# Optimization experiments

Measured on AMD Instinct MI355X. Metric: run time of the kernel, lower is better.

## Reference

```python
import jax, jax.numpy as jnp
import numpy as np

N = 50000   # num_nodes
E = 400000  # random edges (avg degree 8)


def setup_inputs() -> dict:
    key = jax.random.key(0)
    ks = jax.random.split(key, 12)

    def w(k, shape):
        # xavier-ish scaling
        return (jax.random.normal(k, shape, jnp.float32)
                / jnp.sqrt(jnp.float32(shape[0])))

    return {
        "node_emb": jax.random.normal(ks[0], (N, 128), jnp.float32) * 0.05,
        "edge_index": jax.random.randint(ks[1], (2, E), 0, N, dtype=jnp.int32),
        "W1": w(ks[2], (128, 512)), "b1": jnp.zeros((512,), jnp.float32),
        "W2": w(ks[3], (512, 128)), "b2": jnp.zeros((128,), jnp.float32),
        "Wres": w(ks[4], (512, 128)), "bres": jnp.zeros((128,), jnp.float32),
        "Wfc1": w(ks[5], (128, 256)), "bfc1": jnp.zeros((256,), jnp.float32),
        "Wfc2": w(ks[6], (256, 1)), "bfc2": jnp.zeros((1,), jnp.float32),
    }


def reference(node_emb, edge_index, W1, b1, W2, b2, Wres, bres,
              Wfc1, bfc1, Wfc2, bfc2):
    n = node_emb.shape[0]
    loops = jnp.arange(n, dtype=edge_index.dtype)
    # explicit add_self_loops in forward + GCNConv's internal gcn_norm self
    # loops => each node gets TWO self loops (faithful to the torch code).
    src = jnp.concatenate([edge_index[0], loops, loops])
    dst = jnp.concatenate([edge_index[1], loops, loops])

    deg = jax.ops.segment_sum(jnp.ones(src.shape, node_emb.dtype), dst,
                              num_segments=n)
    dinv = jnp.where(deg > 0, jax.lax.rsqrt(deg), 0.0)
    norm = dinv[src] * dinv[dst]  # [Etot]

    def gcn(x, W, b):
        h = x @ W                                    # [N, out]
        msg = h[src] * norm[:, None]                 # gather + scale
        agg = jax.ops.segment_sum(msg, dst, num_segments=n)  # scatter-add
        return agg + b

    x1 = jax.nn.relu(gcn(node_emb, W1, b1))   # [N, 512] (dropout = eval/id)
    x2 = jax.nn.relu(gcn(x1, W2, b2))          # [N, 128]
    x = x2 + x1 @ Wres + bres                  # residual projection
    A = jax.nn.relu(x @ Wfc1 + bfc1) @ Wfc2 + bfc2  # [N, 1]
    return (x, A)
```

## Files before the change

### kernel.cpp

```cpp
#include <hip/hip_runtime.h>


typedef unsigned short u16;
typedef short bf16x8 __attribute__((ext_vector_type(8)));
typedef unsigned short us8 __attribute__((ext_vector_type(8)));
typedef float f32x4 __attribute__((ext_vector_type(4)));

static inline int cdiv_ll(long long a, long long b) { return (int)((a + b - 1) / b); }

__device__ inline float bf2f(u16 u) {
    union { unsigned int i; float f; } v; v.i = ((unsigned int)u) << 16; return v.f;
}
__device__ inline u16 f2bf(float x) {
    union { float f; unsigned int i; } v; v.f = x;
    unsigned int r = v.i + 0x7fffu + ((v.i >> 16) & 1u);
    return (u16)(r >> 16);
}


__global__ __launch_bounds__(256) void setup_kernel(const float* __restrict__ emb,
                                                    const float* __restrict__ W1,
                                                    const float* __restrict__ W2,
                                                    const float* __restrict__ Wres,
                                                    const float* __restrict__ Wfc1,
                                                    const float* __restrict__ bfc2,
                                                    u16* __restrict__ embb,
                                                    u16* __restrict__ W1t,
                                                    u16* __restrict__ Wct,
                                                    u16* __restrict__ Wfc1t,
                                                    int* __restrict__ cnt,
                                                    float* __restrict__ Aout,
                                                    int N) {
    long long r = (long long)blockIdx.x * 256 + threadIdx.x;
    const long long nf2b = (long long)N * 32;
    if (r < nf2b) {
        float4 v = ((const float4*)emb)[r];
        uint2 o;
        o.x = (unsigned)f2bf(v.x) | ((unsigned)f2bf(v.y) << 16);
        o.y = (unsigned)f2bf(v.z) | ((unsigned)f2bf(v.w) << 16);
        ((uint2*)embb)[r] = o;
        return;
    }
    r -= nf2b;
    if (r < 512 * 128) {
        int n = (int)(r / 128), k = (int)(r % 128);
        W1t[r] = f2bf(W1[(size_t)k * 512 + n]);
        return;
    }
    r -= 512 * 128;
    if (r < 256 * 512) {
        int n = (int)(r / 512), k = (int)(r % 512);
        float v = (n < 128) ? W2[(size_t)k * 128 + n] : Wres[(size_t)k * 128 + (n - 128)];
        Wct[r] = f2bf(v);
        return;
    }
    r -= 256 * 512;
    if (r < 256 * 128) {
        int n = (int)(r / 128), k = (int)(r % 128);
        Wfc1t[r] = f2bf(Wfc1[(size_t)k * 256 + n]);
        return;
    }
    r -= 256 * 128;
    if (r < N) { cnt[(int)r] = 0; return; }
    r -= N;
    if (r < N) Aout[(int)r] = bfc2[0];
}


__global__ __launch_bounds__(256) void hist_kernel(const int* __restrict__ dst,
                                                   int* __restrict__ cnt, int E) {
    int e = blockIdx.x * 256 + threadIdx.x;
    if (e < E) atomicAdd(&cnt[dst[e]], 1);
}

__global__ __launch_bounds__(256) void scanA_kernel(const int* __restrict__ cnt,
                                                    int* __restrict__ excl,
                                                    int* __restrict__ bsum, int N) {
    __shared__ int tmp[256];
    int i = blockIdx.x * 256 + threadIdx.x;
    int v = (i < N) ? cnt[i] : 0;
    tmp[threadIdx.x] = v;
    __syncthreads();
    for (int o = 1; o < 256; o <<= 1) {
        int t = (threadIdx.x >= (unsigned)o) ? tmp[threadIdx.x - o] : 0;
        __syncthreads();
        tmp[threadIdx.x] += t;
        __syncthreads();
    }
    if (i < N) excl[i] = tmp[threadIdx.x] - v;
    if (threadIdx.x == 255) bsum[blockIdx.x] = tmp[255];
}

__global__ __launch_bounds__(256) void scanB_kernel(int* __restrict__ bsum, int nb) {
    __shared__ int tmp[256];
    int v = (threadIdx.x < (unsigned)nb) ? bsum[threadIdx.x] : 0;
    tmp[threadIdx.x] = v;
    __syncthreads();
    for (int o = 1; o < 256; o <<= 1) {
        int t = (threadIdx.x >= (unsigned)o) ? tmp[threadIdx.x - o] : 0;
        __syncthreads();
        tmp[threadIdx.x] += t;
        __syncthreads();
    }
    if (threadIdx.x < (unsigned)nb) bsum[threadIdx.x] = tmp[threadIdx.x] - v;
}

__global__ __launch_bounds__(256) void scanC_kernel(const int* __restrict__ excl,
                                                    const int* __restrict__ bsum,
                                                    const int* __restrict__ cnt,
                                                    int* __restrict__ rowptr,
                                                    int* __restrict__ cursor,
                                                    float* __restrict__ dinv,
                                                    int N, int E) {
    int i = blockIdx.x * 256 + threadIdx.x;
    if (i < N) {
        int r = excl[i] + bsum[blockIdx.x];
        rowptr[i] = r;
        cursor[i] = r;
        dinv[i] = rsqrtf((float)cnt[i] + 2.0f);
    }
    if (i == 0) rowptr[N] = E;
}

__global__ __launch_bounds__(256) void fill_kernel(const int* __restrict__ src,
                                                   const int* __restrict__ dst,
                                                   const float* __restrict__ dinv,
                                                   int* __restrict__ cursor,
                                                   int* __restrict__ csr_src,
                                                   float* __restrict__ csr_w, int E) {
    int e = blockIdx.x * 256 + threadIdx.x;
    if (e >= E) return;
    int s = src[e], d = dst[e];
    int idx = atomicAdd(&cursor[d], 1);
    csr_src[idx] = s;
    csr_w[idx] = dinv[s] * dinv[d];
}


#define AGG_EDGE(SR, WR)                                                       \
    {                                                                          \
        unsigned int vv = hp[(size_t)(SR) * 64 + lane];                        \
        ax = fmaf(bf2f((u16)vv), (WR), ax);                                    \
        ay = fmaf(bf2f((u16)(vv >> 16)), (WR), ay);                            \
    }

__device__ inline void agg_row(const unsigned int* __restrict__ hp,
                               const int* __restrict__ rowptr,
                               const int* __restrict__ csr_src,
                               const float* __restrict__ csr_w,
                               const float* __restrict__ dinv,
                               int wid, int lane, float& ax, float& ay) {
    float dv = dinv[wid];
    unsigned int hv = hp[(size_t)wid * 64 + lane];
    float c0 = 2.0f * dv * dv;
    ax = bf2f((u16)hv) * c0;
    ay = bf2f((u16)(hv >> 16)) * c0;
    int e = rowptr[wid], e1 = rowptr[wid + 1];
    for (; e + 7 < e1; e += 8) {
        int s0 = csr_src[e + 0], s1 = csr_src[e + 1], s2 = csr_src[e + 2], s3 = csr_src[e + 3];
        int s4 = csr_src[e + 4], s5 = csr_src[e + 5], s6 = csr_src[e + 6], s7 = csr_src[e + 7];
        float w0 = csr_w[e + 0], w1 = csr_w[e + 1], w2 = csr_w[e + 2], w3 = csr_w[e + 3];
        float w4 = csr_w[e + 4], w5 = csr_w[e + 5], w6 = csr_w[e + 6], w7 = csr_w[e + 7];
        AGG_EDGE(s0, w0); AGG_EDGE(s1, w1); AGG_EDGE(s2, w2); AGG_EDGE(s3, w3);
        AGG_EDGE(s4, w4); AGG_EDGE(s5, w5); AGG_EDGE(s6, w6); AGG_EDGE(s7, w7);
    }
    if (e + 3 < e1) {
        int s0 = csr_src[e + 0], s1 = csr_src[e + 1], s2 = csr_src[e + 2], s3 = csr_src[e + 3];
        float w0 = csr_w[e + 0], w1 = csr_w[e + 1], w2 = csr_w[e + 2], w3 = csr_w[e + 3];
        AGG_EDGE(s0, w0); AGG_EDGE(s1, w1); AGG_EDGE(s2, w2); AGG_EDGE(s3, w3);
        e += 4;
    }
    for (; e < e1; ++e) {
        int s0 = csr_src[e]; float w0 = csr_w[e];
        AGG_EDGE(s0, w0);
    }
}

__global__ __launch_bounds__(256) void aggb_kernel(const u16* __restrict__ hb,
                                                   const int* __restrict__ rowptr,
                                                   const int* __restrict__ csr_src,
                                                   const float* __restrict__ csr_w,
                                                   const float* __restrict__ dinv,
                                                   u16* __restrict__ out, int N) {
    int wid  = (blockIdx.x * blockDim.x + threadIdx.x) >> 6;
    int lane = threadIdx.x & 63;
    if (wid >= N) return;
    float ax, ay;
    agg_row((const unsigned int*)hb, rowptr, csr_src, csr_w, dinv, wid, lane, ax, ay);
    ((unsigned int*)out)[(size_t)wid * 64 + lane] =
        (unsigned)f2bf(ax) | ((unsigned)f2bf(ay) << 16);
}

__global__ __launch_bounds__(256) void aggfin_kernel(const u16* __restrict__ hb,
                                                     const int* __restrict__ rowptr,
                                                     const int* __restrict__ csr_src,
                                                     const float* __restrict__ csr_w,
                                                     const float* __restrict__ dinv,
                                                     const float* __restrict__ b2,
                                                     const float* __restrict__ bres,
                                                     float* __restrict__ xout,
                                                     u16* __restrict__ xb, int N) {
    int wid  = (blockIdx.x * blockDim.x + threadIdx.x) >> 6;
    int lane = threadIdx.x & 63;
    if (wid >= N) return;
    float ax, ay;
    agg_row((const unsigned int*)hb, rowptr, csr_src, csr_w, dinv, wid, lane, ax, ay);
    float2 bb = ((const float2*)b2)[lane];
    float2 rr = ((const float2*)bres)[lane];
    float2 hres = ((float2*)xout)[(size_t)wid * 64 + lane];
    float ox = fmaxf(ax + bb.x, 0.f) + hres.x + rr.x;
    float oy = fmaxf(ay + bb.y, 0.f) + hres.y + rr.y;
    ((float2*)xout)[(size_t)wid * 64 + lane] = make_float2(ox, oy);
    ((unsigned int*)xb)[(size_t)wid * 64 + lane] =
        (unsigned)f2bf(ox) | ((unsigned)f2bf(oy) << 16);
}


template <int MODE, int PIPE>
__global__ __launch_bounds__(512) void mgemm(const u16* __restrict__ A,
                                             const u16* __restrict__ Bt,
                                             int M, int Nn, int K,
                                             const float* __restrict__ bias,
                                             u16* __restrict__ Cb,
                                             float* __restrict__ Cf,
                                             const float* __restrict__ w2) {
    __shared__ u16 As[128][72];
    __shared__ u16 Bs[256][72];
    const int t = threadIdx.x;
    const int bm = blockIdx.y * 128;
    const int bn = blockIdx.x * 256;
    const int w = t >> 6, lane = t & 63;
    const int wm = w >> 2, wn = w & 3;
    const int l15 = lane & 15, lg = lane >> 4;
    const int srow = t >> 3, scol = (t & 7) * 8;

    f32x4 acc[4][4];
#pragma unroll
    for (int i = 0; i < 4; ++i)
#pragma unroll
        for (int j = 0; j < 4; ++j) acc[i][j] = (f32x4)(0.0f);

    us8 ra[2], rb[4];
    if (PIPE) {
#pragma unroll
        for (int i = 0; i < 2; ++i) {
            int row = srow + 64 * i;
            us8 v = (us8)(u16)0;
            if (bm + row < M) v = *(const us8*)(A + (size_t)(bm + row) * K + scol);
            ra[i] = v;
        }
#pragma unroll
        for (int i = 0; i < 4; ++i)
            rb[i] = *(const us8*)(Bt + (size_t)(bn + srow + 64 * i) * K + scol);
    }

    for (int kk = 0; kk < K; kk += 64) {
        if (PIPE) {
#pragma unroll
            for (int i = 0; i < 2; ++i) *(us8*)&As[srow + 64 * i][scol] = ra[i];
#pragma unroll
            for (int i = 0; i < 4; ++i) *(us8*)&Bs[srow + 64 * i][scol] = rb[i];
        } else {
#pragma unroll
            for (int i = 0; i < 2; ++i) {
                int row = srow + 64 * i;
                us8 v = (us8)(u16)0;
                if (bm + row < M)
                    v = *(const us8*)(A + (size_t)(bm + row) * K + kk + scol);
                *(us8*)&As[row][scol] = v;
            }
#pragma unroll
            for (int i = 0; i < 4; ++i) {
                int row = srow + 64 * i;
                *(us8*)&Bs[row][scol] =
                    *(const us8*)(Bt + (size_t)(bn + row) * K + kk + scol);
            }
        }
        __syncthreads();

        if (PIPE && kk + 64 < K) {
#pragma unroll
            for (int i = 0; i < 2; ++i) {
                int row = srow + 64 * i;
                us8 v = (us8)(u16)0;
                if (bm + row < M)
                    v = *(const us8*)(A + (size_t)(bm + row) * K + kk + 64 + scol);
                ra[i] = v;
            }
#pragma unroll
            for (int i = 0; i < 4; ++i)
                rb[i] = *(const us8*)(Bt + (size_t)(bn + srow + 64 * i) * K + kk + 64 + scol);
        }

#pragma unroll
        for (int ks = 0; ks < 2; ++ks) {
            const int ko = 32 * ks + lg * 8;
            bf16x8 bfr[4], afr[4];
#pragma unroll
            for (int fn = 0; fn < 4; ++fn)
                bfr[fn] = *(const bf16x8*)&Bs[64 * wn + 16 * fn + l15][ko];
#pragma unroll
            for (int fm = 0; fm < 4; ++fm)
                afr[fm] = *(const bf16x8*)&As[64 * wm + 16 * fm + l15][ko];
#pragma unroll
            for (int fm = 0; fm < 4; ++fm)
#pragma unroll
                for (int fn = 0; fn < 4; ++fn)
                    acc[fm][fn] = __builtin_amdgcn_mfma_f32_16x16x32_bf16(
                        bfr[fn], afr[fm], acc[fm][fn], 0, 0, 0);
        }
        __syncthreads();
    }

    if (MODE == 3) {
        float4 bl4[4], wl4[4];
#pragma unroll
        for (int fn = 0; fn < 4; ++fn) {
            int c = bn + 64 * wn + 16 * fn + 4 * lg;
            bl4[fn] = *(const float4*)&bias[c];
            wl4[fn] = *(const float4*)&w2[c];
        }
#pragma unroll
        for (int fm = 0; fm < 4; ++fm) {
            float p = 0.f;
#pragma unroll
            for (int fn = 0; fn < 4; ++fn) {
                p += fmaxf(acc[fm][fn][0] + bl4[fn].x, 0.f) * wl4[fn].x;
                p += fmaxf(acc[fm][fn][1] + bl4[fn].y, 0.f) * wl4[fn].y;
                p += fmaxf(acc[fm][fn][2] + bl4[fn].z, 0.f) * wl4[fn].z;
                p += fmaxf(acc[fm][fn][3] + bl4[fn].w, 0.f) * wl4[fn].w;
            }
            p += __shfl_xor(p, 16);
            p += __shfl_xor(p, 32);
            int row = bm + 64 * wm + 16 * fm + l15;
            if (lane < 16 && row < M) atomicAdd(&Cf[row], p);
        }
        return;
    }

#pragma unroll
    for (int fm = 0; fm < 4; ++fm) {
        const int row = bm + 64 * wm + 16 * fm + l15;
        if (row >= M) continue;
#pragma unroll
        for (int fn = 0; fn < 4; ++fn) {
            const int col = bn + 64 * wn + 16 * fn + 4 * lg;
            f32x4 v = acc[fm][fn];
            if (MODE == 1) {
                float4 b4 = *(const float4*)&bias[col];
                float v0 = fmaxf(v[0] + b4.x, 0.f), v1 = fmaxf(v[1] + b4.y, 0.f);
                float v2 = fmaxf(v[2] + b4.z, 0.f), v3 = fmaxf(v[3] + b4.w, 0.f);
                uint2 o;
                o.x = (unsigned)f2bf(v0) | ((unsigned)f2bf(v1) << 16);
                o.y = (unsigned)f2bf(v2) | ((unsigned)f2bf(v3) << 16);
                *(uint2*)(Cb + (size_t)row * Nn + col) = o;
            } else {
                if (col < 128) {
                    uint2 o;
                    o.x = (unsigned)f2bf(v[0]) | ((unsigned)f2bf(v[1]) << 16);
                    o.y = (unsigned)f2bf(v[2]) | ((unsigned)f2bf(v[3]) << 16);
                    *(uint2*)(Cb + (size_t)row * 128 + col) = o;
                } else {
                    *(float4*)(Cf + (size_t)row * 128 + (col - 128)) =
                        make_float4(v[0], v[1], v[2], v[3]);
                }
            }
        }
    }
}


extern "C" void kernel_launch(void* const* d_in, const int* in_sizes, int n_in,
                              void* d_out, int out_size, void* d_ws, size_t ws_size,
                              hipStream_t stream) {
    const float* emb  = (const float*)d_in[0];
    const int*   eidx = (const int*)d_in[1];
    const float* W1   = (const float*)d_in[2];
    const float* b1   = (const float*)d_in[3];
    const float* W2   = (const float*)d_in[4];
    const float* b2   = (const float*)d_in[5];
    const float* Wres = (const float*)d_in[6];
    const float* bres = (const float*)d_in[7];
    const float* Wfc1 = (const float*)d_in[8];
    const float* bfc1 = (const float*)d_in[9];
    const float* Wfc2 = (const float*)d_in[10];
    const float* bfc2 = (const float*)d_in[11];

    const int N = in_sizes[0] / 128;
    const int E = in_sizes[1] / 2;
    const int* srcv = eidx;
    const int* dstv = eidx + E;

    float* out  = (float*)d_out;
    float* xout = out;
    float* Aout = out + (size_t)N * 128;

    char* p = (char*)d_ws;
    float* dinv  = (float*)p;            p += (size_t)N * 4;
    float* csr_w = (float*)p;            p += (size_t)E * 4;
    u16*  embb   = (u16*)p;              p += (size_t)N * 128 * 2;
    u16*  aggEb  = (u16*)p;              p += (size_t)N * 128 * 2;
    u16*  x1b    = (u16*)p;              p += (size_t)N * 512 * 2;
    u16*  h2b    = (u16*)p;              p += (size_t)N * 128 * 2;
    u16*  xb     = (u16*)p;              p += (size_t)N * 128 * 2;
    u16*  W1t    = (u16*)p;              p += (size_t)512 * 128 * 2;
    u16*  Wct    = (u16*)p;              p += (size_t)256 * 512 * 2;
    u16*  Wfc1t  = (u16*)p;              p += (size_t)256 * 128 * 2;
    int*  cnt     = (int*)p;             p += (size_t)N * 4;
    int*  excl    = (int*)p;             p += (size_t)N * 4;
    int*  rowptr  = (int*)p;             p += (size_t)(N + 1) * 4;
    int*  cursor  = (int*)p;             p += (size_t)N * 4;
    int*  bsum    = (int*)p;             p += 256 * 4;
    int*  csr_src = (int*)p;             p += (size_t)E * 4;

    const int T  = 256;
    const int nb = cdiv_ll(N, 256);

    const long long setup_work = (long long)N * 32 + 512 * 128 + 256 * 512
                               + 256 * 128 + (long long)N + (long long)N;
    setup_kernel<<<cdiv_ll(setup_work, T), T, 0, stream>>>(
        emb, W1, W2, Wres, Wfc1, bfc2, embb, W1t, Wct, Wfc1t, cnt, Aout, N);

    hist_kernel<<<cdiv_ll(E, T), T, 0, stream>>>(dstv, cnt, E);
    scanA_kernel<<<nb, T, 0, stream>>>(cnt, excl, bsum, N);
    scanB_kernel<<<1, T, 0, stream>>>(bsum, nb);
    scanC_kernel<<<nb, T, 0, stream>>>(excl, bsum, cnt, rowptr, cursor, dinv, N, E);
    fill_kernel<<<cdiv_ll(E, T), T, 0, stream>>>(srcv, dstv, dinv, cursor, csr_src, csr_w, E);

    aggb_kernel<<<cdiv_ll((long long)N * 64, T), T, 0, stream>>>(
        embb, rowptr, csr_src, csr_w, dinv, aggEb, N);

    mgemm<1, 0><<<dim3(512 / 256, cdiv_ll(N, 128)), 512, 0, stream>>>(
        aggEb, W1t, N, 512, 128, b1, x1b, nullptr, nullptr);

    mgemm<2, 1><<<dim3(1, cdiv_ll(N, 128)), 512, 0, stream>>>(
        x1b, Wct, N, 256, 512, nullptr, h2b, xout, nullptr);

    aggfin_kernel<<<cdiv_ll((long long)N * 64, T), T, 0, stream>>>(
        h2b, rowptr, csr_src, csr_w, dinv, b2, bres, xout, xb, N);

    mgemm<3, 0><<<dim3(1, cdiv_ll(N, 128)), 512, 0, stream>>>(
        xb, Wfc1t, N, 256, 128, bfc1, nullptr, Aout, Wfc2);
}
```

Measured before the change: 198.0 us.

## Chunk feature dimension into 32-column slabs for cache-friendly aggregation gathers

Stores the bf16 node features consumed by both aggregations in a chunked layout, [4][N][32], where each slab holds 32 features for every node. Each aggregation runs as 4 passes, one per slab, with 16 lanes per node. A slab is about 3.2 MB, so the random neighbour gathers in a pass stay within a smaller working set that fits in L2. Setup, the first GEMM's A-loader and the second GEMM's h2 epilogue are all changed to read or write the chunked layout. The cost is that every edge's index and weight is now read four times, and each gather is a shorter 64-byte segment.

```diff
diff --git a/kernel.cpp b/kernel.cpp
--- a/kernel.cpp
+++ b/kernel.cpp
@@ -34,11 +34,13 @@
     long long r = (long long)blockIdx.x * 256 + threadIdx.x;
     const long long nf2b = (long long)N * 32;
     if (r < nf2b) {
+        int node = (int)(r >> 5);
+        int f    = (int)(r & 31) * 4;
         float4 v = ((const float4*)emb)[r];
         uint2 o;
         o.x = (unsigned)f2bf(v.x) | ((unsigned)f2bf(v.y) << 16);
         o.y = (unsigned)f2bf(v.z) | ((unsigned)f2bf(v.w) << 16);
-        ((uint2*)embb)[r] = o;
+        *(uint2*)(embb + ((size_t)(f >> 5) * N + node) * 32 + (f & 31)) = o;
         return;
     }
     r -= nf2b;
@@ -137,86 +139,74 @@
 }
 
 
-#define AGG_EDGE(SR, WR)                                                       \
+#define AGGC_EDGE(SR, WR)                                                      \
     {                                                                          \
-        unsigned int vv = hp[(size_t)(SR) * 64 + lane];                        \
+        unsigned int vv = hp[(size_t)(SR) * 16 + l];                           \
         ax = fmaf(bf2f((u16)vv), (WR), ax);                                    \
         ay = fmaf(bf2f((u16)(vv >> 16)), (WR), ay);                            \
     }
 
-__device__ inline void agg_row(const unsigned int* __restrict__ hp,
-                               const int* __restrict__ rowptr,
-                               const int* __restrict__ csr_src,
-                               const float* __restrict__ csr_w,
-                               const float* __restrict__ dinv,
-                               int wid, int lane, float& ax, float& ay) {
-    float dv = dinv[wid];
-    unsigned int hv = hp[(size_t)wid * 64 + lane];
+template <int FINAL>
+__global__ __launch_bounds__(256) void aggc_kernel(const u16* __restrict__ hb,
+                                                   const int* __restrict__ rowptr,
+                                                   const int* __restrict__ csr_src,
+                                                   const float* __restrict__ csr_w,
+                                                   const float* __restrict__ dinv,
+                                                   const float* __restrict__ b2,
+                                                   const float* __restrict__ bres,
+                                                   float* __restrict__ xout,
+                                                   u16* __restrict__ outb,
+                                                   int N) {
+    const int l = threadIdx.x & 15;
+    const int node = blockIdx.x * 16 + (threadIdx.x >> 4);
+    const int chunk = blockIdx.y;
+    if (node >= N) return;
+    const unsigned int* hp = (const unsigned int*)hb + (size_t)chunk * N * 16;
+
+    float dv = dinv[node];
     float c0 = 2.0f * dv * dv;
-    ax = bf2f((u16)hv) * c0;
-    ay = bf2f((u16)(hv >> 16)) * c0;
-    int e = rowptr[wid], e1 = rowptr[wid + 1];
+    unsigned int hv = hp[(size_t)node * 16 + l];
+    float ax = bf2f((u16)hv) * c0;
+    float ay = bf2f((u16)(hv >> 16)) * c0;
+
+    int e = rowptr[node], e1 = rowptr[node + 1];
     for (; e + 7 < e1; e += 8) {
         int s0 = csr_src[e + 0], s1 = csr_src[e + 1], s2 = csr_src[e + 2], s3 = csr_src[e + 3];
         int s4 = csr_src[e + 4], s5 = csr_src[e + 5], s6 = csr_src[e + 6], s7 = csr_src[e + 7];
         float w0 = csr_w[e + 0], w1 = csr_w[e + 1], w2 = csr_w[e + 2], w3 = csr_w[e + 3];
         float w4 = csr_w[e + 4], w5 = csr_w[e + 5], w6 = csr_w[e + 6], w7 = csr_w[e + 7];
-        AGG_EDGE(s0, w0); AGG_EDGE(s1, w1); AGG_EDGE(s2, w2); AGG_EDGE(s3, w3);
-        AGG_EDGE(s4, w4); AGG_EDGE(s5, w5); AGG_EDGE(s6, w6); AGG_EDGE(s7, w7);
+        AGGC_EDGE(s0, w0); AGGC_EDGE(s1, w1); AGGC_EDGE(s2, w2); AGGC_EDGE(s3, w3);
+        AGGC_EDGE(s4, w4); AGGC_EDGE(s5, w5); AGGC_EDGE(s6, w6); AGGC_EDGE(s7, w7);
     }
     if (e + 3 < e1) {
         int s0 = csr_src[e + 0], s1 = csr_src[e + 1], s2 = csr_src[e + 2], s3 = csr_src[e + 3];
         float w0 = csr_w[e + 0], w1 = csr_w[e + 1], w2 = csr_w[e + 2], w3 = csr_w[e + 3];
-        AGG_EDGE(s0, w0); AGG_EDGE(s1, w1); AGG_EDGE(s2, w2); AGG_EDGE(s3, w3);
+        AGGC_EDGE(s0, w0); AGGC_EDGE(s1, w1); AGGC_EDGE(s2, w2); AGGC_EDGE(s3, w3);
         e += 4;
     }
     for (; e < e1; ++e) {
         int s0 = csr_src[e]; float w0 = csr_w[e];
-        AGG_EDGE(s0, w0);
-    }
-}
-
-__global__ __launch_bounds__(256) void aggb_kernel(const u16* __restrict__ hb,
-                                                   const int* __restrict__ rowptr,
-                                                   const int* __restrict__ csr_src,
-                                                   const float* __restrict__ csr_w,
-                                                   const float* __restrict__ dinv,
-                                                   u16* __restrict__ out, int N) {
-    int wid  = (blockIdx.x * blockDim.x + threadIdx.x) >> 6;
-    int lane = threadIdx.x & 63;
-    if (wid >= N) return;
-    float ax, ay;
-    agg_row((const unsigned int*)hb, rowptr, csr_src, csr_w, dinv, wid, lane, ax, ay);
-    ((unsigned int*)out)[(size_t)wid * 64 + lane] =
-        (unsigned)f2bf(ax) | ((unsigned)f2bf(ay) << 16);
-}
-
-__global__ __launch_bounds__(256) void aggfin_kernel(const u16* __restrict__ hb,
-                                                     const int* __restrict__ rowptr,
-                                                     const int* __restrict__ csr_src,
-                                                     const float* __restrict__ csr_w,
-                                                     const float* __restrict__ dinv,
-                                                     const float* __restrict__ b2,
-                                                     const float* __restrict__ bres,
-                                                     float* __restrict__ xout,
-                                                     u16* __restrict__ xb, int N) {
-    int wid  = (blockIdx.x * blockDim.x + threadIdx.x) >> 6;
-    int lane = threadIdx.x & 63;
-    if (wid >= N) return;
-    float ax, ay;
-    agg_row((const unsigned int*)hb, rowptr, csr_src, csr_w, dinv, wid, lane, ax, ay);
-    float2 bb = ((const float2*)b2)[lane];
-    float2 rr = ((const float2*)bres)[lane];
-    float2 hres = ((float2*)xout)[(size_t)wid * 64 + lane];
-    float ox = fmaxf(ax + bb.x, 0.f) + hres.x + rr.x;
-    float oy = fmaxf(ay + bb.y, 0.f) + hres.y + rr.y;
-    ((float2*)xout)[(size_t)wid * 64 + lane] = make_float2(ox, oy);
-    ((unsigned int*)xb)[(size_t)wid * 64 + lane] =
-        (unsigned)f2bf(ox) | ((unsigned)f2bf(oy) << 16);
-}
-
-
-template <int MODE, int PIPE>
+        AGGC_EDGE(s0, w0);
+    }
+
+    if (FINAL) {
+        int f2 = chunk * 16 + l;
+        float2 bb = ((const float2*)b2)[f2];
+        float2 rr = ((const float2*)bres)[f2];
+        float2 hres = ((float2*)xout)[(size_t)node * 64 + f2];
+        float ox = fmaxf(ax + bb.x, 0.f) + hres.x + rr.x;
+        float oy = fmaxf(ay + bb.y, 0.f) + hres.y + rr.y;
+        ((float2*)xout)[(size_t)node * 64 + f2] = make_float2(ox, oy);
+        ((unsigned int*)outb)[(size_t)node * 64 + f2] =
+            (unsigned)f2bf(ox) | ((unsigned)f2bf(oy) << 16);
+    } else {
+        ((unsigned int*)outb)[((size_t)chunk * N + node) * 16 + l] =
+            (unsigned)f2bf(ax) | ((unsigned)f2bf(ay) << 16);
+    }
+}
+
+
+template <int MODE, int PIPE, int ACHUNK>
 __global__ __launch_bounds__(512) void mgemm(const u16* __restrict__ A,
                                              const u16* __restrict__ Bt,
                                              int M, int Nn, int K,
@@ -234,6 +224,13 @@
     const int l15 = lane & 15, lg = lane >> 4;
     const int srow = t >> 3, scol = (t & 7) * 8;
 
+    auto ald = [&](int grow, int col) -> us8 {
+        if (grow >= M) return (us8)(u16)0;
+        if (ACHUNK)
+            return *(const us8*)(A + ((size_t)(col >> 5) * M + grow) * 32 + (col & 31));
+        return *(const us8*)(A + (size_t)grow * K + col);
+    };
+
     f32x4 acc[4][4];
 #pragma unroll
     for (int i = 0; i < 4; ++i)
@@ -243,12 +240,7 @@
     us8 ra[2], rb[4];
     if (PIPE) {
 #pragma unroll
-        for (int i = 0; i < 2; ++i) {
-            int row = srow + 64 * i;
-            us8 v = (us8)(u16)0;
-            if (bm + row < M) v = *(const us8*)(A + (size_t)(bm + row) * K + scol);
-            ra[i] = v;
-        }
+        for (int i = 0; i < 2; ++i) ra[i] = ald(bm + srow + 64 * i, scol);
 #pragma unroll
         for (int i = 0; i < 4; ++i)
             rb[i] = *(const us8*)(Bt + (size_t)(bn + srow + 64 * i) * K + scol);
@@ -262,13 +254,8 @@
             for (int i = 0; i < 4; ++i) *(us8*)&Bs[srow + 64 * i][scol] = rb[i];
         } else {
 #pragma unroll
-            for (int i = 0; i < 2; ++i) {
-                int row = srow + 64 * i;
-                us8 v = (us8)(u16)0;
-                if (bm + row < M)
-                    v = *(const us8*)(A + (size_t)(bm + row) * K + kk + scol);
-                *(us8*)&As[row][scol] = v;
-            }
+            for (int i = 0; i < 2; ++i)
+                *(us8*)&As[srow + 64 * i][scol] = ald(bm + srow + 64 * i, kk + scol);
 #pragma unroll
             for (int i = 0; i < 4; ++i) {
                 int row = srow + 64 * i;
@@ -280,13 +267,7 @@
 
         if (PIPE && kk + 64 < K) {
 #pragma unroll
-            for (int i = 0; i < 2; ++i) {
-                int row = srow + 64 * i;
-                us8 v = (us8)(u16)0;
-                if (bm + row < M)
-                    v = *(const us8*)(A + (size_t)(bm + row) * K + kk + 64 + scol);
-                ra[i] = v;
-            }
+            for (int i = 0; i < 2; ++i) ra[i] = ald(bm + srow + 64 * i, kk + 64 + scol);
 #pragma unroll
             for (int i = 0; i < 4; ++i)
                 rb[i] = *(const us8*)(Bt + (size_t)(bn + srow + 64 * i) * K + kk + 64 + scol);
@@ -359,7 +340,7 @@
                     uint2 o;
                     o.x = (unsigned)f2bf(v[0]) | ((unsigned)f2bf(v[1]) << 16);
                     o.y = (unsigned)f2bf(v[2]) | ((unsigned)f2bf(v[3]) << 16);
-                    *(uint2*)(Cb + (size_t)row * 128 + col) = o;
+                    *(uint2*)(Cb + ((size_t)(col >> 5) * M + row) * 32 + (col & 31)) = o;
                 } else {
                     *(float4*)(Cf + (size_t)row * 128 + (col - 128)) =
                         make_float4(v[0], v[1], v[2], v[3]);
@@ -427,18 +408,19 @@
     scanC_kernel<<<nb, T, 0, stream>>>(excl, bsum, cnt, rowptr, cursor, dinv, N, E);
     fill_kernel<<<cdiv_ll(E, T), T, 0, stream>>>(srcv, dstv, dinv, cursor, csr_src, csr_w, E);
 
-    aggb_kernel<<<cdiv_ll((long long)N * 64, T), T, 0, stream>>>(
-        embb, rowptr, csr_src, csr_w, dinv, aggEb, N);
-
-    mgemm<1, 0><<<dim3(512 / 256, cdiv_ll(N, 128)), 512, 0, stream>>>(
+    dim3 aggGrid(cdiv_ll(N, 16), 4);
+    aggc_kernel<0><<<aggGrid, T, 0, stream>>>(
+        embb, rowptr, csr_src, csr_w, dinv, nullptr, nullptr, nullptr, aggEb, N);
+
+    mgemm<1, 0, 1><<<dim3(512 / 256, cdiv_ll(N, 128)), 512, 0, stream>>>(
         aggEb, W1t, N, 512, 128, b1, x1b, nullptr, nullptr);
 
-    mgemm<2, 1><<<dim3(1, cdiv_ll(N, 128)), 512, 0, stream>>>(
+    mgemm<2, 1, 0><<<dim3(1, cdiv_ll(N, 128)), 512, 0, stream>>>(
         x1b, Wct, N, 256, 512, nullptr, h2b, xout, nullptr);
 
-    aggfin_kernel<<<cdiv_ll((long long)N * 64, T), T, 0, stream>>>(
+    aggc_kernel<1><<<aggGrid, T, 0, stream>>>(
         h2b, rowptr, csr_src, csr_w, dinv, b2, bres, xout, xb, N);
 
-    mgemm<3, 0><<<dim3(1, cdiv_ll(N, 128)), 512, 0, stream>>>(
+    mgemm<3, 0, 0><<<dim3(1, cdiv_ll(N, 128)), 512, 0, stream>>>(
         xb, Wfc1t, N, 256, 128, bfc1, nullptr, Aout, Wfc2);
 }
```

Result: slower. 212.7 us (+7.4%).

## Fuse layer-1 GEMM into combined W2/Wres GEMM keeping x1 in LDS

Applied to the files above, without the earlier changes.

The first-layer GEMM (aggE·W1 + bias, relu) and the second GEMM (x1·[W2|Wres]) are merged into one kernel. Each block computes a 128x128 chunk of x1 in shared memory and immediately consumes it, so the N×512 bf16 x1 intermediate is never written to or read back from global memory. The scan kernels are also merged: each block reduces the preceding block sums itself, which removes the single-block scanB launch. The cost is about 136KB of dynamic LDS per block, which lowers occupancy, and there is no global-load pipelining in the fused loop.

```diff
diff --git a/kernel.cpp b/kernel.cpp
--- a/kernel.cpp
+++ b/kernel.cpp
@@ -91,30 +91,25 @@
     if (threadIdx.x == 255) bsum[blockIdx.x] = tmp[255];
 }
 
-__global__ __launch_bounds__(256) void scanB_kernel(int* __restrict__ bsum, int nb) {
+__global__ __launch_bounds__(256) void scanC2_kernel(const int* __restrict__ excl,
+                                                     const int* __restrict__ bsum,
+                                                     const int* __restrict__ cnt,
+                                                     int* __restrict__ rowptr,
+                                                     int* __restrict__ cursor,
+                                                     float* __restrict__ dinv,
+                                                     int N, int E) {
     __shared__ int tmp[256];
-    int v = (threadIdx.x < (unsigned)nb) ? bsum[threadIdx.x] : 0;
-    tmp[threadIdx.x] = v;
+    int t = threadIdx.x;
+    tmp[t] = (t < (int)blockIdx.x) ? bsum[t] : 0;
     __syncthreads();
-    for (int o = 1; o < 256; o <<= 1) {
-        int t = (threadIdx.x >= (unsigned)o) ? tmp[threadIdx.x - o] : 0;
-        __syncthreads();
-        tmp[threadIdx.x] += t;
-        __syncthreads();
-    }
-    if (threadIdx.x < (unsigned)nb) bsum[threadIdx.x] = tmp[threadIdx.x] - v;
-}
-
-__global__ __launch_bounds__(256) void scanC_kernel(const int* __restrict__ excl,
-                                                    const int* __restrict__ bsum,
-                                                    const int* __restrict__ cnt,
-                                                    int* __restrict__ rowptr,
-                                                    int* __restrict__ cursor,
-                                                    float* __restrict__ dinv,
-                                                    int N, int E) {
-    int i = blockIdx.x * 256 + threadIdx.x;
+    for (int o = 128; o; o >>= 1) {
+        if (t < o) tmp[t] += tmp[t + o];
+        __syncthreads();
+    }
+    int pre = tmp[0];
+    int i = blockIdx.x * 256 + t;
     if (i < N) {
-        int r = excl[i] + bsum[blockIdx.x];
+        int r = excl[i] + pre;
         rowptr[i] = r;
         cursor[i] = r;
         dinv[i] = rsqrtf((float)cnt[i] + 2.0f);
@@ -216,156 +211,219 @@
 }
 
 
-template <int MODE, int PIPE>
-__global__ __launch_bounds__(512) void mgemm(const u16* __restrict__ A,
-                                             const u16* __restrict__ Bt,
-                                             int M, int Nn, int K,
-                                             const float* __restrict__ bias,
-                                             u16* __restrict__ Cb,
-                                             float* __restrict__ Cf,
-                                             const float* __restrict__ w2) {
-    __shared__ u16 As[128][72];
-    __shared__ u16 Bs[256][72];
+__global__ __launch_bounds__(512) void mgemm12(const u16* __restrict__ aggE,
+                                               const u16* __restrict__ W1t,
+                                               const u16* __restrict__ Wct,
+                                               const float* __restrict__ b1,
+                                               int M,
+                                               u16* __restrict__ h2b,
+                                               float* __restrict__ xout) {
+    extern __shared__ u16 smem[];
+    u16* Ag  = smem;
+    u16* Ws  = Ag + 128 * 136;
+    u16* X1s = Ws + 256 * 136;
+    const int LD = 136;
+
     const int t = threadIdx.x;
-    const int bm = blockIdx.y * 128;
-    const int bn = blockIdx.x * 256;
+    const int bm = blockIdx.x * 128;
     const int w = t >> 6, lane = t & 63;
     const int wm = w >> 2, wn = w & 3;
     const int l15 = lane & 15, lg = lane >> 4;
-    const int srow = t >> 3, scol = (t & 7) * 8;
-
-    f32x4 acc[4][4];
+
+#pragma unroll
+    for (int i = 0; i < 4; ++i) {
+        int c = t + 512 * i;
+        int row = c >> 4, cs = (c & 15) * 8;
+        us8 v = (us8)(u16)0;
+        if (bm + row < M) v = *(const us8*)(aggE + (size_t)(bm + row) * 128 + cs);
+        *(us8*)&Ag[row * LD + cs] = v;
+    }
+
+    f32x4 acc2[4][4];
 #pragma unroll
     for (int i = 0; i < 4; ++i)
 #pragma unroll
-        for (int j = 0; j < 4; ++j) acc[i][j] = (f32x4)(0.0f);
-
-    us8 ra[2], rb[4];
-    if (PIPE) {
-#pragma unroll
-        for (int i = 0; i < 2; ++i) {
-            int row = srow + 64 * i;
-            us8 v = (us8)(u16)0;
-            if (bm + row < M) v = *(const us8*)(A + (size_t)(bm + row) * K + scol);
-            ra[i] = v;
-        }
+        for (int j = 0; j < 4; ++j) acc2[i][j] = (f32x4)(0.0f);
+
+    for (int p = 0; p < 4; ++p) {
+        __syncthreads();
+#pragma unroll
+        for (int i = 0; i < 4; ++i) {
+            int c = t + 512 * i;
+            int row = c >> 4, cs = (c & 15) * 8;
+            *(us8*)&Ws[row * LD + cs] =
+                *(const us8*)(W1t + (size_t)(128 * p + row) * 128 + cs);
+        }
+        __syncthreads();
+
+        f32x4 acc1[4][2];
 #pragma unroll
         for (int i = 0; i < 4; ++i)
-            rb[i] = *(const us8*)(Bt + (size_t)(bn + srow + 64 * i) * K + scol);
-    }
-
-    for (int kk = 0; kk < K; kk += 64) {
-        if (PIPE) {
-#pragma unroll
-            for (int i = 0; i < 2; ++i) *(us8*)&As[srow + 64 * i][scol] = ra[i];
-#pragma unroll
-            for (int i = 0; i < 4; ++i) *(us8*)&Bs[srow + 64 * i][scol] = rb[i];
-        } else {
-#pragma unroll
-            for (int i = 0; i < 2; ++i) {
-                int row = srow + 64 * i;
-                us8 v = (us8)(u16)0;
-                if (bm + row < M)
-                    v = *(const us8*)(A + (size_t)(bm + row) * K + kk + scol);
-                *(us8*)&As[row][scol] = v;
-            }
-#pragma unroll
-            for (int i = 0; i < 4; ++i) {
-                int row = srow + 64 * i;
-                *(us8*)&Bs[row][scol] =
-                    *(const us8*)(Bt + (size_t)(bn + row) * K + kk + scol);
-            }
-        }
-        __syncthreads();
-
-        if (PIPE && kk + 64 < K) {
-#pragma unroll
-            for (int i = 0; i < 2; ++i) {
-                int row = srow + 64 * i;
-                us8 v = (us8)(u16)0;
-                if (bm + row < M)
-                    v = *(const us8*)(A + (size_t)(bm + row) * K + kk + 64 + scol);
-                ra[i] = v;
-            }
-#pragma unroll
-            for (int i = 0; i < 4; ++i)
-                rb[i] = *(const us8*)(Bt + (size_t)(bn + srow + 64 * i) * K + kk + 64 + scol);
-        }
-
-#pragma unroll
-        for (int ks = 0; ks < 2; ++ks) {
+#pragma unroll
+            for (int j = 0; j < 2; ++j) acc1[i][j] = (f32x4)(0.0f);
+#pragma unroll
+        for (int ks = 0; ks < 4; ++ks) {
             const int ko = 32 * ks + lg * 8;
-            bf16x8 bfr[4], afr[4];
-#pragma unroll
-            for (int fn = 0; fn < 4; ++fn)
-                bfr[fn] = *(const bf16x8*)&Bs[64 * wn + 16 * fn + l15][ko];
-#pragma unroll
-            for (int fm = 0; fm < 4; ++fm)
-                afr[fm] = *(const bf16x8*)&As[64 * wm + 16 * fm + l15][ko];
-#pragma unroll
-            for (int fm = 0; fm < 4; ++fm)
-#pragma unroll
-                for (int fn = 0; fn < 4; ++fn)
-                    acc[fm][fn] = __builtin_amdgcn_mfma_f32_16x16x32_bf16(
-                        bfr[fn], afr[fm], acc[fm][fn], 0, 0, 0);
-        }
-        __syncthreads();
-    }
-
-    if (MODE == 3) {
-        float4 bl4[4], wl4[4];
-#pragma unroll
-        for (int fn = 0; fn < 4; ++fn) {
-            int c = bn + 64 * wn + 16 * fn + 4 * lg;
-            bl4[fn] = *(const float4*)&bias[c];
-            wl4[fn] = *(const float4*)&w2[c];
-        }
+            bf16x8 wfr[2], afr[4];
+#pragma unroll
+            for (int fn = 0; fn < 2; ++fn)
+                wfr[fn] = *(const bf16x8*)&Ws[(32 * wn + 16 * fn + l15) * LD + ko];
+#pragma unroll
+            for (int fm = 0; fm < 4; ++fm)
+                afr[fm] = *(const bf16x8*)&Ag[(64 * wm + 16 * fm + l15) * LD + ko];
+#pragma unroll
+            for (int fm = 0; fm < 4; ++fm)
+#pragma unroll
+                for (int fn = 0; fn < 2; ++fn)
+                    acc1[fm][fn] = __builtin_amdgcn_mfma_f32_16x16x32_bf16(
+                        wfr[fn], afr[fm], acc1[fm][fn], 0, 0, 0);
+        }
+        __syncthreads();
+
 #pragma unroll
         for (int fm = 0; fm < 4; ++fm) {
-            float p = 0.f;
-#pragma unroll
-            for (int fn = 0; fn < 4; ++fn) {
-                p += fmaxf(acc[fm][fn][0] + bl4[fn].x, 0.f) * wl4[fn].x;
-                p += fmaxf(acc[fm][fn][1] + bl4[fn].y, 0.f) * wl4[fn].y;
-                p += fmaxf(acc[fm][fn][2] + bl4[fn].z, 0.f) * wl4[fn].z;
-                p += fmaxf(acc[fm][fn][3] + bl4[fn].w, 0.f) * wl4[fn].w;
-            }
-            p += __shfl_xor(p, 16);
-            p += __shfl_xor(p, 32);
-            int row = bm + 64 * wm + 16 * fm + l15;
-            if (lane < 16 && row < M) atomicAdd(&Cf[row], p);
-        }
-        return;
-    }
-
-#pragma unroll
-    for (int fm = 0; fm < 4; ++fm) {
-        const int row = bm + 64 * wm + 16 * fm + l15;
-        if (row >= M) continue;
-#pragma unroll
-        for (int fn = 0; fn < 4; ++fn) {
-            const int col = bn + 64 * wn + 16 * fn + 4 * lg;
-            f32x4 v = acc[fm][fn];
-            if (MODE == 1) {
-                float4 b4 = *(const float4*)&bias[col];
+#pragma unroll
+            for (int fn = 0; fn < 2; ++fn) {
+                int col1 = 32 * wn + 16 * fn + 4 * lg;
+                float4 b4 = *(const float4*)&b1[128 * p + col1];
+                f32x4 v = acc1[fm][fn];
                 float v0 = fmaxf(v[0] + b4.x, 0.f), v1 = fmaxf(v[1] + b4.y, 0.f);
                 float v2 = fmaxf(v[2] + b4.z, 0.f), v3 = fmaxf(v[3] + b4.w, 0.f);
                 uint2 o;
                 o.x = (unsigned)f2bf(v0) | ((unsigned)f2bf(v1) << 16);
                 o.y = (unsigned)f2bf(v2) | ((unsigned)f2bf(v3) << 16);
-                *(uint2*)(Cb + (size_t)row * Nn + col) = o;
+                *(uint2*)&X1s[(64 * wm + 16 * fm + l15) * LD + col1] = o;
+            }
+        }
+#pragma unroll
+        for (int i = 0; i < 8; ++i) {
+            int c = t + 512 * i;
+            int row = c >> 4, cs = (c & 15) * 8;
+            *(us8*)&Ws[row * LD + cs] =
+                *(const us8*)(Wct + (size_t)row * 512 + 128 * p + cs);
+        }
+        __syncthreads();
+
+#pragma unroll
+        for (int ks = 0; ks < 4; ++ks) {
+            const int ko = 32 * ks + lg * 8;
+            bf16x8 wfr[4], xfr[4];
+#pragma unroll
+            for (int fn = 0; fn < 4; ++fn)
+                wfr[fn] = *(const bf16x8*)&Ws[(64 * wn + 16 * fn + l15) * LD + ko];
+#pragma unroll
+            for (int fm = 0; fm < 4; ++fm)
+                xfr[fm] = *(const bf16x8*)&X1s[(64 * wm + 16 * fm + l15) * LD + ko];
+#pragma unroll
+            for (int fm = 0; fm < 4; ++fm)
+#pragma unroll
+                for (int fn = 0; fn < 4; ++fn)
+                    acc2[fm][fn] = __builtin_amdgcn_mfma_f32_16x16x32_bf16(
+                        wfr[fn], xfr[fm], acc2[fm][fn], 0, 0, 0);
+        }
+    }
+
+#pragma unroll
+    for (int fm = 0; fm < 4; ++fm) {
+        const int row = bm + 64 * wm + 16 * fm + l15;
+        if (row >= M) continue;
+#pragma unroll
+        for (int fn = 0; fn < 4; ++fn) {
+            const int col = 64 * wn + 16 * fn + 4 * lg;
+            f32x4 v = acc2[fm][fn];
+            if (col < 128) {
+                uint2 o;
+                o.x = (unsigned)f2bf(v[0]) | ((unsigned)f2bf(v[1]) << 16);
+                o.y = (unsigned)f2bf(v[2]) | ((unsigned)f2bf(v[3]) << 16);
+                *(uint2*)(h2b + (size_t)row * 128 + col) = o;
             } else {
-                if (col < 128) {
-                    uint2 o;
-                    o.x = (unsigned)f2bf(v[0]) | ((unsigned)f2bf(v[1]) << 16);
-                    o.y = (unsigned)f2bf(v[2]) | ((unsigned)f2bf(v[3]) << 16);
-                    *(uint2*)(Cb + (size_t)row * 128 + col) = o;
-                } else {
-                    *(float4*)(Cf + (size_t)row * 128 + (col - 128)) =
-                        make_float4(v[0], v[1], v[2], v[3]);
-                }
+                *(float4*)(xout + (size_t)row * 128 + (col - 128)) =
+                    make_float4(v[0], v[1], v[2], v[3]);
             }
         }
+    }
+}
+
+
+__global__ __launch_bounds__(512) void head_gemm(const u16* __restrict__ A,
+                                                 const u16* __restrict__ Bt,
+                                                 int M,
+                                                 const float* __restrict__ bias,
+                                                 const float* __restrict__ w2,
+                                                 float* __restrict__ Cf) {
+    __shared__ u16 As[128][72];
+    __shared__ u16 Bs[256][72];
+    const int t = threadIdx.x;
+    const int bm = blockIdx.x * 128;
+    const int w = t >> 6, lane = t & 63;
+    const int wm = w >> 2, wn = w & 3;
+    const int l15 = lane & 15, lg = lane >> 4;
+    const int srow = t >> 3, scol = (t & 7) * 8;
+    const int K = 128;
+
+    f32x4 acc[4][4];
+#pragma unroll
+    for (int i = 0; i < 4; ++i)
+#pragma unroll
+        for (int j = 0; j < 4; ++j) acc[i][j] = (f32x4)(0.0f);
+
+    for (int kk = 0; kk < K; kk += 64) {
+#pragma unroll
+        for (int i = 0; i < 2; ++i) {
+            int row = srow + 64 * i;
+            us8 v = (us8)(u16)0;
+            if (bm + row < M)
+                v = *(const us8*)(A + (size_t)(bm + row) * K + kk + scol);
+            *(us8*)&As[row][scol] = v;
+        }
+#pragma unroll
+        for (int i = 0; i < 4; ++i) {
+            int row = srow + 64 * i;
+            *(us8*)&Bs[row][scol] =
+                *(const us8*)(Bt + (size_t)row * K + kk + scol);
+        }
+        __syncthreads();
+#pragma unroll
+        for (int ks = 0; ks < 2; ++ks) {
+            const int ko = 32 * ks + lg * 8;
+            bf16x8 bfr[4], afr[4];
+#pragma unroll
+            for (int fn = 0; fn < 4; ++fn)
+                bfr[fn] = *(const bf16x8*)&Bs[64 * wn + 16 * fn + l15][ko];
+#pragma unroll
+            for (int fm = 0; fm < 4; ++fm)
+                afr[fm] = *(const bf16x8*)&As[64 * wm + 16 * fm + l15][ko];
+#pragma unroll
+            for (int fm = 0; fm < 4; ++fm)
+#pragma unroll
+                for (int fn = 0; fn < 4; ++fn)
+                    acc[fm][fn] = __builtin_amdgcn_mfma_f32_16x16x32_bf16(
+                        bfr[fn], afr[fm], acc[fm][fn], 0, 0, 0);
+        }
+        __syncthreads();
+    }
+
+    float4 bl4[4], wl4[4];
+#pragma unroll
+    for (int fn = 0; fn < 4; ++fn) {
+        int c = 64 * wn + 16 * fn + 4 * lg;
+        bl4[fn] = *(const float4*)&bias[c];
+        wl4[fn] = *(const float4*)&w2[c];
+    }
+#pragma unroll
+    for (int fm = 0; fm < 4; ++fm) {
+        float p = 0.f;
+#pragma unroll
+        for (int fn = 0; fn < 4; ++fn) {
+            p += fmaxf(acc[fm][fn][0] + bl4[fn].x, 0.f) * wl4[fn].x;
+            p += fmaxf(acc[fm][fn][1] + bl4[fn].y, 0.f) * wl4[fn].y;
+            p += fmaxf(acc[fm][fn][2] + bl4[fn].z, 0.f) * wl4[fn].z;
+            p += fmaxf(acc[fm][fn][3] + bl4[fn].w, 0.f) * wl4[fn].w;
+        }
+        p += __shfl_xor(p, 16);
+        p += __shfl_xor(p, 32);
+        int row = bm + 64 * wm + 16 * fm + l15;
+        if (lane < 16 && row < M) atomicAdd(&Cf[row], p);
     }
 }
 
@@ -400,7 +458,6 @@
     float* csr_w = (float*)p;            p += (size_t)E * 4;
     u16*  embb   = (u16*)p;              p += (size_t)N * 128 * 2;
     u16*  aggEb  = (u16*)p;              p += (size_t)N * 128 * 2;
-    u16*  x1b    = (u16*)p;              p += (size_t)N * 512 * 2;
     u16*  h2b    = (u16*)p;              p += (size_t)N * 128 * 2;
     u16*  xb     = (u16*)p;              p += (size_t)N * 128 * 2;
     u16*  W1t    = (u16*)p;              p += (size_t)512 * 128 * 2;
@@ -423,22 +480,19 @@
 
     hist_kernel<<<cdiv_ll(E, T), T, 0, stream>>>(dstv, cnt, E);
     scanA_kernel<<<nb, T, 0, stream>>>(cnt, excl, bsum, N);
-    scanB_kernel<<<1, T, 0, stream>>>(bsum, nb);
-    scanC_kernel<<<nb, T, 0, stream>>>(excl, bsum, cnt, rowptr, cursor, dinv, N, E);
+    scanC2_kernel<<<nb, T, 0, stream>>>(excl, bsum, cnt, rowptr, cursor, dinv, N, E);
     fill_kernel<<<cdiv_ll(E, T), T, 0, stream>>>(srcv, dstv, dinv, cursor, csr_src, csr_w, E);
 
     aggb_kernel<<<cdiv_ll((long long)N * 64, T), T, 0, stream>>>(
         embb, rowptr, csr_src, csr_w, dinv, aggEb, N);
 
-    mgemm<1, 0><<<dim3(512 / 256, cdiv_ll(N, 128)), 512, 0, stream>>>(
-        aggEb, W1t, N, 512, 128, b1, x1b, nullptr, nullptr);
-
-    mgemm<2, 1><<<dim3(1, cdiv_ll(N, 128)), 512, 0, stream>>>(
-        x1b, Wct, N, 256, 512, nullptr, h2b, xout, nullptr);
+    const size_t lds12 = (size_t)(128 * 136 + 256 * 136 + 128 * 136) * sizeof(u16);
+    mgemm12<<<cdiv_ll(N, 128), 512, lds12, stream>>>(
+        aggEb, W1t, Wct, b1, N, h2b, xout);
 
     aggfin_kernel<<<cdiv_ll((long long)N * 64, T), T, 0, stream>>>(
         h2b, rowptr, csr_src, csr_w, dinv, b2, bres, xout, xb, N);
 
-    mgemm<3, 0><<<dim3(1, cdiv_ll(N, 128)), 512, 0, stream>>>(
-        xb, Wfc1t, N, 256, 128, bfc1, nullptr, Aout, Wfc2);
-}
+    head_gemm<<<cdiv_ll(N, 128), 512, 0, stream>>>(
+        xb, Wfc1t, N, bfc1, Wfc2, Aout);
+}
```

New measurement: 178.3 us. 1.11x faster.
